# Optimization experiments

Measured on AMD Instinct MI355X. Metric: run time of the kernel, lower is better.

## Reference

```python
import jax, jax.numpy as jnp
import numpy as np

B, S, E, H, Dh = 1, 2048, 1024, 16, 64


def setup_inputs() -> dict:
    key = jax.random.key(0)
    ks = jax.random.split(key, 9)
    sc = 0.02
    return {
        "x": jax.random.normal(ks[0], (B, S, E), jnp.float32),
        "Wq": jax.random.normal(ks[1], (H, E, Dh), jnp.float32) * sc,
        "bq": jax.random.normal(ks[2], (H, Dh), jnp.float32) * sc,
        "Wk": jax.random.normal(ks[3], (H, E, Dh), jnp.float32) * sc,
        "bk": jax.random.normal(ks[4], (H, Dh), jnp.float32) * sc,
        "Wv": jax.random.normal(ks[5], (H, E, Dh), jnp.float32) * sc,
        "bv": jax.random.normal(ks[6], (H, Dh), jnp.float32) * sc,
        "Wo": jax.random.normal(ks[7], (E, E), jnp.float32) * sc,
        "bo": jax.random.normal(ks[8], (E,), jnp.float32) * sc,
    }


def reference(x, Wq, bq, Wk, bk, Wv, bv, Wo, bo):
    # Per-head projections (stacked): [B,S,E] x [H,E,Dh] -> [B,H,S,Dh]
    q = jnp.einsum("bse,hed->bhsd", x, Wq) + bq[None, :, None, :]
    k = jnp.einsum("bse,hed->bhsd", x, Wk) + bk[None, :, None, :]
    v = jnp.einsum("bse,hed->bhsd", x, Wv) + bv[None, :, None, :]
    scores = jnp.einsum("bhsd,bhtd->bhst", q, k) / np.sqrt(Dh).astype(np.float32)
    causal = jnp.tril(jnp.ones((S, S), dtype=bool))  # [S,S]
    scores = jnp.where(causal[None, None], scores, -jnp.inf)
    attn = jax.nn.softmax(scores, axis=-1)  # attn_dropout p=0 -> identity
    out = jnp.einsum("bhst,bhtd->bhsd", attn, v)
    # concat heads in head order: [B,S,H*Dh]
    out = out.transpose(0, 2, 1, 3).reshape(B, S, H * Dh)
    return out @ Wo.T if False else jnp.einsum("bsf,ef->bse", out, Wo.T.T * 0 + Wo) if False else out @ Wo.swapaxes(0, 1) * 0 + (jnp.einsum("bsf,fe->bse", out, Wo) + bo)
```

## Files before the change

kernel.cpp:

```cpp
#include <hip/hip_runtime.h>

#define S_LEN 2048
#define E_DIM 1024
#define NH 16
#define DH 64

typedef __bf16 v8bf __attribute__((ext_vector_type(8)));
typedef float f32x4 __attribute__((ext_vector_type(4)));
typedef unsigned short u16x4 __attribute__((ext_vector_type(4)));
typedef unsigned short u16x8 __attribute__((ext_vector_type(8)));

__device__ __align__(16) unsigned short g_Xb[S_LEN * E_DIM];
__device__ __align__(16) unsigned short g_WT[3 * E_DIM * E_DIM];
__device__ __align__(16) unsigned short g_WoT[E_DIM * E_DIM];
__device__ __align__(16) unsigned short g_Qb[NH * S_LEN * DH];
__device__ __align__(16) unsigned short g_Kb[NH * S_LEN * DH];
__device__ __align__(16) unsigned short g_Vt[NH * DH * S_LEN];
__device__ __align__(16) unsigned short g_AO[S_LEN * E_DIM];

__device__ inline unsigned short f2bf(float f) {
    unsigned int u = __float_as_uint(f);
    u += 0x7FFF + ((u >> 16) & 1);
    return (unsigned short)(u >> 16);
}
__device__ inline f32x4 mfma16(v8bf a, v8bf b, f32x4 c) {
    return __builtin_amdgcn_mfma_f32_16x16x32_bf16(a, b, c, 0, 0, 0);
}
#define SWZ(v, pat) __int_as_float(__builtin_amdgcn_ds_swizzle(__float_as_int(v), (pat)))

typedef __attribute__((address_space(3))) unsigned int lds_u32;
typedef __attribute__((address_space(1))) const unsigned int glb_u32;
__device__ inline void async_cp16(const unsigned short* g, unsigned short* l) {
    __builtin_amdgcn_global_load_lds((glb_u32*)g, (lds_u32*)l, 16, 0, 0);
}

__global__ __launch_bounds__(256) void prep(const float* __restrict__ X,
                                            const float* __restrict__ Wq,
                                            const float* __restrict__ Wk,
                                            const float* __restrict__ Wv,
                                            const float* __restrict__ Wo) {
    __shared__ __align__(16) unsigned short lds[64 * 72];
    const int b = blockIdx.x;
    const int t = threadIdx.x;
    if (b < 2048) {
        int i = b * 256 + t;
        f32x4 v = reinterpret_cast<const f32x4*>(X)[i];
        u16x4 o = {f2bf(v.x), f2bf(v.y), f2bf(v.z), f2bf(v.w)};
        reinterpret_cast<u16x4*>(g_Xb)[i] = o;
    } else if (b < 2304) {
        int bb = b - 2048;
        const int h = bb >> 4;
        const int e0 = (bb & 15) * 64;
        const float* srcs[3] = {Wq, Wk, Wv};
#pragma unroll
        for (int tn = 0; tn < 3; tn++) {
            const float* W = srcs[tn] + h * 65536;
#pragma unroll
            for (int p = 0; p < 4; p++) {
                int e = p * 16 + (t >> 4);
                int d = (t & 15) * 4;
                f32x4 v = *reinterpret_cast<const f32x4*>(&W[(e0 + e) * 64 + d]);
                lds[(d + 0) * 72 + e] = f2bf(v.x);
                lds[(d + 1) * 72 + e] = f2bf(v.y);
                lds[(d + 2) * 72 + e] = f2bf(v.z);
                lds[(d + 3) * 72 + e] = f2bf(v.w);
            }
            __syncthreads();
#pragma unroll
            for (int p = 0; p < 2; p++) {
                int d = p * 32 + (t >> 3);
                int ec = (t & 7) * 8;
                u16x8 o = *reinterpret_cast<const u16x8*>(&lds[d * 72 + ec]);
                *reinterpret_cast<u16x8*>(&g_WT[(tn * 1024 + h * 64 + d) * E_DIM + e0 + ec]) = o;
            }
            __syncthreads();
        }
    } else {
        int bb = b - 2304;
        const int f0 = (bb >> 4) * 64;
        const int e0 = (bb & 15) * 64;
#pragma unroll
        for (int p = 0; p < 4; p++) {
            int f = p * 16 + (t >> 4);
            int e = (t & 15) * 4;
            f32x4 v = *reinterpret_cast<const f32x4*>(&Wo[(f0 + f) * E_DIM + e0 + e]);
            lds[(e + 0) * 72 + f] = f2bf(v.x);
            lds[(e + 1) * 72 + f] = f2bf(v.y);
            lds[(e + 2) * 72 + f] = f2bf(v.z);
            lds[(e + 3) * 72 + f] = f2bf(v.w);
        }
        __syncthreads();
#pragma unroll
        for (int p = 0; p < 2; p++) {
            int e = p * 32 + (t >> 3);
            int fc = (t & 7) * 8;
            u16x8 o = *reinterpret_cast<const u16x8*>(&lds[e * 72 + fc]);
            *reinterpret_cast<u16x8*>(&g_WoT[(e0 + e) * E_DIM + f0 + fc]) = o;
        }
    }
}

__global__ __launch_bounds__(256) void qkv_gemm(const float* __restrict__ bq,
                                                const float* __restrict__ bk,
                                                const float* __restrict__ bv) {
    __shared__ __align__(16) unsigned short lds[12288];
    unsigned short* lA = lds;
    unsigned short* lB = lds + 8192;
    const int t = threadIdx.x;
    const int wave = t >> 6;
    const int lane = t & 63;
    const int m = lane & 15, quad = lane >> 4;
    const int s0 = blockIdx.x * 128;
    const int n0 = blockIdx.y * 64;

    const int rl = t >> 3;
    const int cx = (t & 7) ^ (rl & 7);
    const int axor = m & 7;

    f32x4 acc[2][4];
#pragma unroll
    for (int i = 0; i < 2; i++)
#pragma unroll
        for (int j = 0; j < 4; j++) acc[i][j] = (f32x4){0.f, 0.f, 0.f, 0.f};

    const unsigned short* lAr0 = lA + (wave * 32 + m) * 64;
    const unsigned short* lAr1 = lA + (wave * 32 + 16 + m) * 64;

    for (int k0 = 0; k0 < E_DIM; k0 += 64) {
        const unsigned short* ga = g_Xb + (s0 + rl) * E_DIM + k0 + cx * 8;
        async_cp16(ga,              lA + wave * 512);
        async_cp16(ga + 32 * E_DIM, lA + 2048 + wave * 512);
        async_cp16(ga + 64 * E_DIM, lA + 4096 + wave * 512);
        async_cp16(ga + 96 * E_DIM, lA + 6144 + wave * 512);
        const unsigned short* gb = g_WT + (n0 + rl) * E_DIM + k0 + cx * 8;
        async_cp16(gb,              lB + wave * 512);
        async_cp16(gb + 32 * E_DIM, lB + 2048 + wave * 512);
        __syncthreads();
#pragma unroll
        for (int ks = 0; ks < 2; ks++) {
            const int ch = ((ks * 4 + quad) ^ axor) * 8;
            v8bf a0 = *reinterpret_cast<const v8bf*>(lAr0 + ch);
            v8bf a1 = *reinterpret_cast<const v8bf*>(lAr1 + ch);
#pragma unroll
            for (int j = 0; j < 4; j++) {
                v8bf bfr = *reinterpret_cast<const v8bf*>(lB + (j * 16 + m) * 64 + ch);
                acc[0][j] = mfma16(a0, bfr, acc[0][j]);
                acc[1][j] = mfma16(a1, bfr, acc[1][j]);
            }
        }
        __syncthreads();
    }

    const int tensor = n0 >> 10;
    const int nn0 = n0 & 1023;
    const int hh = nn0 >> 6;
    const float* bb = tensor == 0 ? bq : (tensor == 1 ? bk : bv);
    float bias[4];
#pragma unroll
    for (int j = 0; j < 4; j++) bias[j] = bb[nn0 + j * 16 + m];

    if (tensor < 2) {
#pragma unroll
        for (int i = 0; i < 2; i++)
#pragma unroll
            for (int j = 0; j < 4; j++)
#pragma unroll
                for (int r = 0; r < 4; r++) {
                    int sl = wave * 32 + i * 16 + quad * 4 + r;
                    int nl = j * 16 + m;
                    lds[sl * 72 + nl] = f2bf(acc[i][j][r] + bias[j]);
                }
        __syncthreads();
        unsigned short* dst = (tensor == 0 ? g_Qb : g_Kb) + (hh * S_LEN + s0) * DH;
#pragma unroll
        for (int p = 0; p < 4; p++) {
            int row = p * 32 + (t >> 3);
            int c = t & 7;
            u16x8 v = *reinterpret_cast<const u16x8*>(&lds[row * 72 + c * 8]);
            *reinterpret_cast<u16x8*>(&dst[row * DH + c * 8]) = v;
        }
    } else {
#pragma unroll
        for (int i = 0; i < 2; i++)
#pragma unroll
            for (int j = 0; j < 4; j++)
#pragma unroll
                for (int r = 0; r < 4; r++) {
                    int sl = wave * 32 + i * 16 + quad * 4 + r;
                    int nl = j * 16 + m;
                    lds[nl * 136 + sl] = f2bf(acc[i][j][r] + bias[j]);
                }
        __syncthreads();
#pragma unroll
        for (int p = 0; p < 4; p++) {
            int nl = p * 16 + (t >> 4);
            int sc = t & 15;
            u16x8 v = *reinterpret_cast<const u16x8*>(&lds[nl * 136 + sc * 8]);
            *reinterpret_cast<u16x8*>(&g_Vt[(hh * DH + nl) * S_LEN + s0 + sc * 8]) = v;
        }
    }
}

__global__ __launch_bounds__(256) void flash_attn() {
    __shared__ __align__(16) unsigned char smem[24576];
    unsigned short* plds = (unsigned short*)smem;
    float* comb = (float*)smem;
    const int t = threadIdx.x;
    const int wave = t >> 6, lane = t & 63;
    const int m = lane & 15, quad = lane >> 4;
    const int h = blockIdx.x & 15;
    const int j = blockIdx.x >> 4;
    const int sA0 = j * 16;
    const int sB0 = 2032 - j * 16;

    const unsigned short* Qh = g_Qb + h * S_LEN * DH;
    const unsigned short* Kh = g_Kb + h * S_LEN * DH;
    const unsigned short* Vh = g_Vt + h * DH * S_LEN;

    v8bf aqA0 = *reinterpret_cast<const v8bf*>(Qh + (sA0 + m) * DH + quad * 8);
    v8bf aqA1 = *reinterpret_cast<const v8bf*>(Qh + (sA0 + m) * DH + 32 + quad * 8);
    v8bf aqB0 = *reinterpret_cast<const v8bf*>(Qh + (sB0 + m) * DH + quad * 8);
    v8bf aqB1 = *reinterpret_cast<const v8bf*>(Qh + (sB0 + m) * DH + 32 + quad * 8);

    f32x4 oA[4], oB[4];
#pragma unroll
    for (int i = 0; i < 4; i++) { oA[i] = (f32x4){0.f,0.f,0.f,0.f}; oB[i] = (f32x4){0.f,0.f,0.f,0.f}; }
    float lsA[4] = {0.f,0.f,0.f,0.f}, lsB[4] = {0.f,0.f,0.f,0.f};

    const float SC = 0.125f * 1.44269504088896f;
    unsigned short* pw = plds + wave * 2304;

    for (int t0 = wave * 64; t0 < sB0 + 16; t0 += 256) {
        const bool doA = (t0 < sA0 + 16);
        v8bf kf[4][2];
#pragma unroll
        for (int ct = 0; ct < 4; ct++) {
            const unsigned short* kp = Kh + (t0 + ct * 16 + m) * DH + quad * 8;
            kf[ct][0] = *reinterpret_cast<const v8bf*>(kp);
            kf[ct][1] = *reinterpret_cast<const v8bf*>(kp + 32);
        }
        f32x4 sB[4];
#pragma unroll
        for (int ct = 0; ct < 4; ct++) {
            sB[ct] = (f32x4){0.f,0.f,0.f,0.f};
            sB[ct] = mfma16(aqB0, kf[ct][0], sB[ct]);
            sB[ct] = mfma16(aqB1, kf[ct][1], sB[ct]);
        }
        f32x4 sA[4];
        if (doA) {
#pragma unroll
            for (int ct = 0; ct < 4; ct++) {
                sA[ct] = (f32x4){0.f,0.f,0.f,0.f};
                sA[ct] = mfma16(aqA0, kf[ct][0], sA[ct]);
                sA[ct] = mfma16(aqA1, kf[ct][1], sA[ct]);
            }
        }
#pragma unroll
        for (int ct = 0; ct < 4; ct++) {
            int colbase = t0 + ct * 16;
            int col = colbase + m;
            if (colbase + 15 > sB0) {
#pragma unroll
                for (int r = 0; r < 4; r++)
                    if (col > sB0 + quad * 4 + r) sB[ct][r] = -3e38f;
            }
            if (doA && colbase + 15 > sA0) {
#pragma unroll
                for (int r = 0; r < 4; r++)
                    if (col > sA0 + quad * 4 + r) sA[ct][r] = -3e38f;
            }
        }
        v8bf vf[4][2];
#pragma unroll
        for (int dt = 0; dt < 4; dt++) {
            const unsigned short* vp = Vh + (dt * 16 + m) * S_LEN + t0 + quad * 8;
            vf[dt][0] = *reinterpret_cast<const v8bf*>(vp);
            vf[dt][1] = *reinterpret_cast<const v8bf*>(vp + 32);
        }
#pragma unroll
        for (int ct = 0; ct < 4; ct++)
#pragma unroll
            for (int r = 0; r < 4; r++)
                sB[ct][r] = __builtin_amdgcn_exp2f(sB[ct][r] * SC);
#pragma unroll
        for (int r = 0; r < 4; r++)
            lsB[r] += (sB[0][r] + sB[1][r]) + (sB[2][r] + sB[3][r]);
#pragma unroll
        for (int ct = 0; ct < 4; ct++)
#pragma unroll
            for (int r = 0; r < 4; r++)
                pw[(16 + quad * 4 + r) * 72 + ct * 16 + m] = f2bf(sB[ct][r]);
        if (doA) {
#pragma unroll
            for (int ct = 0; ct < 4; ct++)
#pragma unroll
                for (int r = 0; r < 4; r++)
                    sA[ct][r] = __builtin_amdgcn_exp2f(sA[ct][r] * SC);
#pragma unroll
            for (int r = 0; r < 4; r++)
                lsA[r] += (sA[0][r] + sA[1][r]) + (sA[2][r] + sA[3][r]);
#pragma unroll
            for (int ct = 0; ct < 4; ct++)
#pragma unroll
                for (int r = 0; r < 4; r++)
                    pw[(quad * 4 + r) * 72 + ct * 16 + m] = f2bf(sA[ct][r]);
        }
        __builtin_amdgcn_s_waitcnt(0xC07F);
        v8bf apB0 = *reinterpret_cast<const v8bf*>(pw + (16 + m) * 72 + quad * 8);
        v8bf apB1 = *reinterpret_cast<const v8bf*>(pw + (16 + m) * 72 + 32 + quad * 8);
#pragma unroll
        for (int dt = 0; dt < 4; dt++) {
            oB[dt] = mfma16(apB0, vf[dt][0], oB[dt]);
            oB[dt] = mfma16(apB1, vf[dt][1], oB[dt]);
        }
        if (doA) {
            v8bf apA0 = *reinterpret_cast<const v8bf*>(pw + m * 72 + quad * 8);
            v8bf apA1 = *reinterpret_cast<const v8bf*>(pw + m * 72 + 32 + quad * 8);
#pragma unroll
            for (int dt = 0; dt < 4; dt++) {
                oA[dt] = mfma16(apA0, vf[dt][0], oA[dt]);
                oA[dt] = mfma16(apA1, vf[dt][1], oA[dt]);
            }
        }
    }

    float* cw = comb + (wave * 64 + lane) * 24;
    __syncthreads();
#pragma unroll
    for (int dt = 0; dt < 4; dt++) *reinterpret_cast<f32x4*>(cw + dt * 4) = oA[dt];
    *reinterpret_cast<f32x4*>(cw + 16) = (f32x4){lsA[0], lsA[1], lsA[2], lsA[3]};
    __syncthreads();
    {
        f32x4 oAt = (f32x4){0.f,0.f,0.f,0.f}, l4 = (f32x4){0.f,0.f,0.f,0.f};
#pragma unroll
        for (int w = 0; w < 4; w++) {
            const float* cr = comb + (w * 64 + lane) * 24;
            oAt += *reinterpret_cast<const f32x4*>(cr + wave * 4);
            l4  += *reinterpret_cast<const f32x4*>(cr + 16);
        }
#pragma unroll
        for (int r = 0; r < 4; r++) {
            float a = l4[r];
            a += SWZ(a, 0x041F); a += SWZ(a, 0x081F);
            a += SWZ(a, 0x101F); a += SWZ(a, 0x201F);
            float inv = 1.0f / a;
            g_AO[(sA0 + quad * 4 + r) * E_DIM + h * 64 + wave * 16 + m] = f2bf(oAt[r] * inv);
        }
    }
    __syncthreads();
#pragma unroll
    for (int dt = 0; dt < 4; dt++) *reinterpret_cast<f32x4*>(cw + dt * 4) = oB[dt];
    *reinterpret_cast<f32x4*>(cw + 16) = (f32x4){lsB[0], lsB[1], lsB[2], lsB[3]};
    __syncthreads();
    {
        f32x4 oBt = (f32x4){0.f,0.f,0.f,0.f}, l4 = (f32x4){0.f,0.f,0.f,0.f};
#pragma unroll
        for (int w = 0; w < 4; w++) {
            const float* cr = comb + (w * 64 + lane) * 24;
            oBt += *reinterpret_cast<const f32x4*>(cr + wave * 4);
            l4  += *reinterpret_cast<const f32x4*>(cr + 16);
        }
#pragma unroll
        for (int r = 0; r < 4; r++) {
            float a = l4[r];
            a += SWZ(a, 0x041F); a += SWZ(a, 0x081F);
            a += SWZ(a, 0x101F); a += SWZ(a, 0x201F);
            float inv = 1.0f / a;
            g_AO[(sB0 + quad * 4 + r) * E_DIM + h * 64 + wave * 16 + m] = f2bf(oBt[r] * inv);
        }
    }
}

__global__ __launch_bounds__(256) void out_gemm(const float* __restrict__ bo,
                                                float* __restrict__ OUT) {
    __shared__ __align__(16) unsigned short lds[8192];
    unsigned short* lA = lds;
    unsigned short* lB = lds + 4096;
    const int t = threadIdx.x;
    const int wave = t >> 6;
    const int lane = t & 63;
    const int m = lane & 15, quad = lane >> 4;
    const int wr = (wave >> 1) * 32, wc = (wave & 1) * 32;
    const int s0 = blockIdx.x * 64;
    const int n0 = blockIdx.y * 64;

    const int rl = t >> 3;
    const int cx = (t & 7) ^ (rl & 7);
    const int axor = m & 7;

    f32x4 acc[2][2];
#pragma unroll
    for (int i = 0; i < 2; i++)
#pragma unroll
        for (int j = 0; j < 2; j++) acc[i][j] = (f32x4){0.f, 0.f, 0.f, 0.f};

    for (int k0 = 0; k0 < E_DIM; k0 += 64) {
        const unsigned short* ga = g_AO + (s0 + rl) * E_DIM + k0 + cx * 8;
        async_cp16(ga,              lA + wave * 512);
        async_cp16(ga + 32 * E_DIM, lA + 2048 + wave * 512);
        const unsigned short* gb = g_WoT + (n0 + rl) * E_DIM + k0 + cx * 8;
        async_cp16(gb,              lB + wave * 512);
        async_cp16(gb + 32 * E_DIM, lB + 2048 + wave * 512);
        __syncthreads();
#pragma unroll
        for (int ks = 0; ks < 2; ks++) {
            const int ch = ((ks * 4 + quad) ^ axor) * 8;
            v8bf a0 = *reinterpret_cast<const v8bf*>(lA + (wr + m) * 64 + ch);
            v8bf a1 = *reinterpret_cast<const v8bf*>(lA + (wr + 16 + m) * 64 + ch);
#pragma unroll
            for (int j = 0; j < 2; j++) {
                v8bf bfr = *reinterpret_cast<const v8bf*>(lB + (wc + j * 16 + m) * 64 + ch);
                acc[0][j] = mfma16(a0, bfr, acc[0][j]);
                acc[1][j] = mfma16(a1, bfr, acc[1][j]);
            }
        }
        __syncthreads();
    }
#pragma unroll
    for (int i = 0; i < 2; i++)
#pragma unroll
        for (int j = 0; j < 2; j++) {
            int e = n0 + wc + j * 16 + m;
            float bias = bo[e];
#pragma unroll
            for (int r = 0; r < 4; r++) {
                int s = s0 + wr + i * 16 + quad * 4 + r;
                OUT[s * E_DIM + e] = acc[i][j][r] + bias;
            }
        }
}

extern "C" void kernel_launch(void* const* d_in, const int* in_sizes, int n_in,
                              void* d_out, int out_size, void* d_ws, size_t ws_size,
                              hipStream_t stream) {
    (void)in_sizes; (void)n_in; (void)out_size; (void)d_ws; (void)ws_size;
    const float* x  = (const float*)d_in[0];
    const float* Wq = (const float*)d_in[1];
    const float* bq = (const float*)d_in[2];
    const float* Wk = (const float*)d_in[3];
    const float* bk = (const float*)d_in[4];
    const float* Wv = (const float*)d_in[5];
    const float* bv = (const float*)d_in[6];
    const float* Wo = (const float*)d_in[7];
    const float* bo = (const float*)d_in[8];
    float* out = (float*)d_out;

    hipLaunchKernelGGL(prep,       dim3(2560),   dim3(256), 0, stream, x, Wq, Wk, Wv, Wo);
    hipLaunchKernelGGL(qkv_gemm,   dim3(16, 48), dim3(256), 0, stream, bq, bk, bv);
    hipLaunchKernelGGL(flash_attn, dim3(1024),   dim3(256), 0, stream);
    hipLaunchKernelGGL(out_gemm,   dim3(32, 16), dim3(256), 0, stream, bo, out);
}
```

Measured before the change: 180.5 us.

## Pair adjacent query tiles per block and compute softmax row sums with MFMA

Each block now handles two adjacent 16-row query tiles (a 32-row tile T), with tiles ordered in a zigzag across blocks for load balance. The old scheme paired a short early tile with a long late tile. Adjacent tiles share almost all key/value loads, so the doA branch is nearly always taken and work per block becomes uneven, which the ordering tries to even out. Row sums of P are computed by an MFMA against a ones vector using the bf16-rounded P, which removes the per-lane scalar adds and cross-lane swizzle reductions. The bf16 conversion also uses the packed HIP intrinsic.

```diff
diff --git a/kernel.cpp b/kernel.cpp
--- a/kernel.cpp
+++ b/kernel.cpp
@@ -1,4 +1,5 @@
 #include <hip/hip_runtime.h>
+#include <hip/hip_bf16.h>
 
 #define S_LEN 2048
 #define E_DIM 1024
@@ -26,7 +27,6 @@
 __device__ inline f32x4 mfma16(v8bf a, v8bf b, f32x4 c) {
     return __builtin_amdgcn_mfma_f32_16x16x32_bf16(a, b, c, 0, 0, 0);
 }
-#define SWZ(v, pat) __int_as_float(__builtin_amdgcn_ds_swizzle(__float_as_int(v), (pat)))
 
 typedef __attribute__((address_space(3))) unsigned int lds_u32;
 typedef __attribute__((address_space(1))) const unsigned int glb_u32;
@@ -209,29 +209,34 @@
     const int wave = t >> 6, lane = t & 63;
     const int m = lane & 15, quad = lane >> 4;
     const int h = blockIdx.x & 15;
-    const int j = blockIdx.x >> 4;
-    const int sA0 = j * 16;
-    const int sB0 = 2032 - j * 16;
+    const int Tp = blockIdx.x >> 4;
+    const int qq = Tp >> 4, tt = Tp & 15;
+    const int T = (qq == 0) ? tt : (qq == 1) ? 31 - tt : (qq == 2) ? 32 + tt : 63 - tt;
+    const int s0 = T * 32;
 
     const unsigned short* Qh = g_Qb + h * S_LEN * DH;
     const unsigned short* Kh = g_Kb + h * S_LEN * DH;
     const unsigned short* Vh = g_Vt + h * DH * S_LEN;
 
-    v8bf aqA0 = *reinterpret_cast<const v8bf*>(Qh + (sA0 + m) * DH + quad * 8);
-    v8bf aqA1 = *reinterpret_cast<const v8bf*>(Qh + (sA0 + m) * DH + 32 + quad * 8);
-    v8bf aqB0 = *reinterpret_cast<const v8bf*>(Qh + (sB0 + m) * DH + quad * 8);
-    v8bf aqB1 = *reinterpret_cast<const v8bf*>(Qh + (sB0 + m) * DH + 32 + quad * 8);
+    v8bf aqA0 = *reinterpret_cast<const v8bf*>(Qh + (s0 + m) * DH + quad * 8);
+    v8bf aqA1 = *reinterpret_cast<const v8bf*>(Qh + (s0 + m) * DH + 32 + quad * 8);
+    v8bf aqB0 = *reinterpret_cast<const v8bf*>(Qh + (s0 + 16 + m) * DH + quad * 8);
+    v8bf aqB1 = *reinterpret_cast<const v8bf*>(Qh + (s0 + 16 + m) * DH + 32 + quad * 8);
 
     f32x4 oA[4], oB[4];
 #pragma unroll
     for (int i = 0; i < 4; i++) { oA[i] = (f32x4){0.f,0.f,0.f,0.f}; oB[i] = (f32x4){0.f,0.f,0.f,0.f}; }
-    float lsA[4] = {0.f,0.f,0.f,0.f}, lsB[4] = {0.f,0.f,0.f,0.f};
+    f32x4 laccA = (f32x4){0.f,0.f,0.f,0.f}, laccB = (f32x4){0.f,0.f,0.f,0.f};
+
+    v8bf ones;
+#pragma unroll
+    for (int i = 0; i < 8; i++) ones[i] = (__bf16)1.0f;
 
     const float SC = 0.125f * 1.44269504088896f;
     unsigned short* pw = plds + wave * 2304;
 
-    for (int t0 = wave * 64; t0 < sB0 + 16; t0 += 256) {
-        const bool doA = (t0 < sA0 + 16);
+    for (int t0 = wave * 64; t0 < s0 + 32; t0 += 256) {
+        const bool doA = (t0 < s0 + 16);
         v8bf kf[4][2];
 #pragma unroll
         for (int ct = 0; ct < 4; ct++) {
@@ -259,15 +264,15 @@
         for (int ct = 0; ct < 4; ct++) {
             int colbase = t0 + ct * 16;
             int col = colbase + m;
-            if (colbase + 15 > sB0) {
+            if (colbase + 15 > s0 + 16) {
 #pragma unroll
                 for (int r = 0; r < 4; r++)
-                    if (col > sB0 + quad * 4 + r) sB[ct][r] = -3e38f;
-            }
-            if (doA && colbase + 15 > sA0) {
+                    if (col > s0 + 16 + quad * 4 + r) sB[ct][r] = -3e38f;
+            }
+            if (doA && colbase + 15 > s0) {
 #pragma unroll
                 for (int r = 0; r < 4; r++)
-                    if (col > sA0 + quad * 4 + r) sA[ct][r] = -3e38f;
+                    if (col > s0 + quad * 4 + r) sA[ct][r] = -3e38f;
             }
         }
         v8bf vf[4][2];
@@ -278,32 +283,32 @@
             vf[dt][1] = *reinterpret_cast<const v8bf*>(vp + 32);
         }
 #pragma unroll
-        for (int ct = 0; ct < 4; ct++)
+        for (int ct = 0; ct < 4; ct++) {
 #pragma unroll
             for (int r = 0; r < 4; r++)
                 sB[ct][r] = __builtin_amdgcn_exp2f(sB[ct][r] * SC);
-#pragma unroll
-        for (int r = 0; r < 4; r++)
-            lsB[r] += (sB[0][r] + sB[1][r]) + (sB[2][r] + sB[3][r]);
-#pragma unroll
-        for (int ct = 0; ct < 4; ct++)
-#pragma unroll
-            for (int r = 0; r < 4; r++)
-                pw[(16 + quad * 4 + r) * 72 + ct * 16 + m] = f2bf(sB[ct][r]);
+            __hip_bfloat162 p01 = __float22bfloat162_rn(make_float2(sB[ct][0], sB[ct][1]));
+            __hip_bfloat162 p23 = __float22bfloat162_rn(make_float2(sB[ct][2], sB[ct][3]));
+            unsigned short* pb = pw + (16 + quad * 4) * 72 + ct * 16 + m;
+            pb[0]       = *reinterpret_cast<unsigned short*>(&p01.x);
+            pb[72]      = *reinterpret_cast<unsigned short*>(&p01.y);
+            pb[144]     = *reinterpret_cast<unsigned short*>(&p23.x);
+            pb[216]     = *reinterpret_cast<unsigned short*>(&p23.y);
+        }
         if (doA) {
 #pragma unroll
-            for (int ct = 0; ct < 4; ct++)
+            for (int ct = 0; ct < 4; ct++) {
 #pragma unroll
                 for (int r = 0; r < 4; r++)
                     sA[ct][r] = __builtin_amdgcn_exp2f(sA[ct][r] * SC);
-#pragma unroll
-            for (int r = 0; r < 4; r++)
-                lsA[r] += (sA[0][r] + sA[1][r]) + (sA[2][r] + sA[3][r]);
-#pragma unroll
-            for (int ct = 0; ct < 4; ct++)
-#pragma unroll
-                for (int r = 0; r < 4; r++)
-                    pw[(quad * 4 + r) * 72 + ct * 16 + m] = f2bf(sA[ct][r]);
+                __hip_bfloat162 p01 = __float22bfloat162_rn(make_float2(sA[ct][0], sA[ct][1]));
+                __hip_bfloat162 p23 = __float22bfloat162_rn(make_float2(sA[ct][2], sA[ct][3]));
+                unsigned short* pa = pw + (quad * 4) * 72 + ct * 16 + m;
+                pa[0]   = *reinterpret_cast<unsigned short*>(&p01.x);
+                pa[72]  = *reinterpret_cast<unsigned short*>(&p01.y);
+                pa[144] = *reinterpret_cast<unsigned short*>(&p23.x);
+                pa[216] = *reinterpret_cast<unsigned short*>(&p23.y);
+            }
         }
         __builtin_amdgcn_s_waitcnt(0xC07F);
         v8bf apB0 = *reinterpret_cast<const v8bf*>(pw + (16 + m) * 72 + quad * 8);
@@ -313,6 +318,8 @@
             oB[dt] = mfma16(apB0, vf[dt][0], oB[dt]);
             oB[dt] = mfma16(apB1, vf[dt][1], oB[dt]);
         }
+        laccB = mfma16(apB0, ones, laccB);
+        laccB = mfma16(apB1, ones, laccB);
         if (doA) {
             v8bf apA0 = *reinterpret_cast<const v8bf*>(pw + m * 72 + quad * 8);
             v8bf apA1 = *reinterpret_cast<const v8bf*>(pw + m * 72 + 32 + quad * 8);
@@ -321,6 +328,8 @@
                 oA[dt] = mfma16(apA0, vf[dt][0], oA[dt]);
                 oA[dt] = mfma16(apA1, vf[dt][1], oA[dt]);
             }
+            laccA = mfma16(apA0, ones, laccA);
+            laccA = mfma16(apA1, ones, laccA);
         }
     }
 
@@ -328,7 +337,7 @@
     __syncthreads();
 #pragma unroll
     for (int dt = 0; dt < 4; dt++) *reinterpret_cast<f32x4*>(cw + dt * 4) = oA[dt];
-    *reinterpret_cast<f32x4*>(cw + 16) = (f32x4){lsA[0], lsA[1], lsA[2], lsA[3]};
+    *reinterpret_cast<f32x4*>(cw + 16) = laccA;
     __syncthreads();
     {
         f32x4 oAt = (f32x4){0.f,0.f,0.f,0.f}, l4 = (f32x4){0.f,0.f,0.f,0.f};
@@ -340,17 +349,14 @@
         }
 #pragma unroll
         for (int r = 0; r < 4; r++) {
-            float a = l4[r];
-            a += SWZ(a, 0x041F); a += SWZ(a, 0x081F);
-            a += SWZ(a, 0x101F); a += SWZ(a, 0x201F);
-            float inv = 1.0f / a;
-            g_AO[(sA0 + quad * 4 + r) * E_DIM + h * 64 + wave * 16 + m] = f2bf(oAt[r] * inv);
+            float inv = 1.0f / l4[r];
+            g_AO[(s0 + quad * 4 + r) * E_DIM + h * 64 + wave * 16 + m] = f2bf(oAt[r] * inv);
         }
     }
     __syncthreads();
 #pragma unroll
     for (int dt = 0; dt < 4; dt++) *reinterpret_cast<f32x4*>(cw + dt * 4) = oB[dt];
-    *reinterpret_cast<f32x4*>(cw + 16) = (f32x4){lsB[0], lsB[1], lsB[2], lsB[3]};
+    *reinterpret_cast<f32x4*>(cw + 16) = laccB;
     __syncthreads();
     {
         f32x4 oBt = (f32x4){0.f,0.f,0.f,0.f}, l4 = (f32x4){0.f,0.f,0.f,0.f};
@@ -362,11 +368,8 @@
         }
 #pragma unroll
         for (int r = 0; r < 4; r++) {
-            float a = l4[r];
-            a += SWZ(a, 0x041F); a += SWZ(a, 0x081F);
-            a += SWZ(a, 0x101F); a += SWZ(a, 0x201F);
-            float inv = 1.0f / a;
-            g_AO[(sB0 + quad * 4 + r) * E_DIM + h * 64 + wave * 16 + m] = f2bf(oBt[r] * inv);
+            float inv = 1.0f / l4[r];
+            g_AO[(s0 + 16 + quad * 4 + r) * E_DIM + h * 64 + wave * 16 + m] = f2bf(oBt[r] * inv);
         }
     }
 }
```

Measured after the change: 167.5 us. 7.2% less time.
